# Optimization experiments

Measured on AMD Instinct MI355X. Metric: run time of the kernel, lower is better.

## Reference

```python
import jax, jax.numpy as jnp
import numpy as np

N = 100000   # nodes
E = 1600000  # edges
IN = 128     # input_dim
H = 64       # hidden_dim
OUT = 2      # output_dim
G = 64       # number of graphs in the batch


def setup_inputs() -> dict:
    key = jax.random.key(0)
    ks = jax.random.split(key, 12)
    x = jax.random.normal(ks[0], (N, IN), dtype=jnp.float32)
    edge_index = jax.random.randint(ks[1], (2, E), 0, N, dtype=jnp.int64)
    batch = jnp.sort(jax.random.randint(ks[2], (N,), 0, G, dtype=jnp.int64))
    s = 0.05
    return {
        "x": x,
        "edge_index": edge_index,
        "batch": batch,
        "W1": jax.random.normal(ks[3], (IN, H), dtype=jnp.float32) * s,
        "b1": jnp.zeros((H,), dtype=jnp.float32),
        "W2": jax.random.normal(ks[4], (H, H), dtype=jnp.float32) * s,
        "b2": jnp.zeros((H,), dtype=jnp.float32),
        "W3": jax.random.normal(ks[5], (H, H), dtype=jnp.float32) * s,
        "b3": jnp.zeros((H,), dtype=jnp.float32),
        "Wm1": jax.random.normal(ks[6], (H, H), dtype=jnp.float32) * s,
        "bm1": jnp.zeros((H,), dtype=jnp.float32),
        "Wm2": jax.random.normal(ks[7], (H, OUT), dtype=jnpp.float32) * s if False else jax.random.normal(ks[7], (H, OUT), dtype=jnp.float32) * s,
        "bm2": jnp.zeros((OUT,), dtype=jnp.float32),
    }


def _gcn_conv(x, W, b, src, dst, norm, n_nodes):
    # PyG GCNConv: h = x @ W; message = norm * h[src]; scatter-add at dst; + bias
    h = x @ W                                  # [N, H]
    msg = h[src] * norm[:, None]               # [E+N, H] gather + scale
    out = jax.ops.segment_sum(msg, dst, num_segments=n_nodes)
    return out + b


def reference(x, edge_index, batch, W1, b1, W2, b2, W3, b3, Wm1, bm1, Wm2, bm2):
    n = x.shape[0]
    # add self-loops (PyG GCNConv default add_self_loops=True)
    loop = jnp.arange(n, dtype=edge_index.dtype)
    src = jnp.concatenate([edge_index[0], loop])
    dst = jnp.concatenate([edge_index[1], loop])
    # symmetric normalization deg^-1/2 (deg over target nodes, incl. self-loops)
    deg = jax.ops.segment_sum(jnp.ones_like(dst, dtype=x.dtype), dst, num_segments=n)
    dinv = jnp.where(deg > 0, jax.lax.rsqrt(deg), 0.0)
    norm = dinv[src] * dinv[dst]               # [E+N]

    h = jax.nn.relu(_gcn_conv(x, W1, b1, src, dst, norm, n))   # dropout: eval -> identity
    h = jax.nn.relu(_gcn_conv(h, W2, b2, src, dst, norm, n))
    h = jax.nn.relu(_gcn_conv(h, W3, b3, src, dst, norm, n))

    # global_mean_pool over batch ids
    sums = jax.ops.segment_sum(h, batch, num_segments=G)       # [G, H]
    cnts = jax.ops.segment_sum(jnp.ones((n,), dtype=h.dtype), batch, num_segments=G)
    pooled = sums / jnp.maximum(cnts, 1.0)[:, None]

    # MLP head: Linear -> ReLU -> (Dropout eval) -> Linear
    z = jax.nn.relu(pooled @ Wm1 + bm1)
    return z @ Wm2 + bm2                                       # [G, OUT]
```

## Files before the change

kernel.cpp:

```cpp
#include <hip/hip_runtime.h>
#include <hip/hip_bf16.h>

#define NNODES 100000
#define NEDGES 1600000
#define IND 128
#define HD 64
#define OUTD 2
#define NG 64
#define BINSHIFT 9
#define BINSZ 512
#define BSTRIDE 12288
#define PB 256

typedef __attribute__((ext_vector_type(8))) short short8v;
typedef __attribute__((ext_vector_type(4))) float floatx4;

static __device__ __forceinline__ unsigned short f2bf(float f) {
    __hip_bfloat16 h = __float2bfloat16(f);
    return *(unsigned short*)&h;
}
static __device__ __forceinline__ float bf2f(unsigned short u) {
    __hip_bfloat16 h = *(__hip_bfloat16*)&u;
    return __bfloat162float(h);
}

__global__ __launch_bounds__(1024) void binP_kernel(const int* __restrict__ src,
                                                    const int* __restrict__ dst,
                                                    int* __restrict__ binCount,
                                                    unsigned int* __restrict__ binned,
                                                    int E, int nbins) {
    __shared__ int lh[256];
    __shared__ int lbase[256];
    int t = threadIdx.x;
    if (t < 256) lh[t] = 0;
    __syncthreads();
    int ebpb = (E + PB - 1) / PB;
    int e0 = blockIdx.x * ebpb;
    int e1 = min(e0 + ebpb, E);
    int dcache[8];
    int ec = 0;
    for (int e = e0 + t; e < e1; e += 1024) {
        int d = dst[e];
        dcache[ec++] = d;
        atomicAdd(&lh[d >> BINSHIFT], 1);
    }
    __syncthreads();
    if (t < nbins) {
        int c = lh[t];
        if (c > 0) lbase[t] = atomicAdd(&binCount[t], c);
        lh[t] = 0;
    }
    __syncthreads();
    ec = 0;
    for (int e = e0 + t; e < e1; e += 1024) {
        int d = dcache[ec++];
        int b = d >> BINSHIFT;
        int idx = atomicAdd(&lh[b], 1);
        binned[(size_t)b * BSTRIDE + lbase[b] + idx] =
            ((unsigned int)(d & (BINSZ - 1)) << 17) | (unsigned int)src[e];
    }
}

__global__ __launch_bounds__(1024) void binHD_kernel(const unsigned int* __restrict__ binned,
                                                     const int* __restrict__ binCount,
                                                     float* __restrict__ dinv,
                                                     unsigned int* __restrict__ rowinfo,
                                                     int* __restrict__ ssrc, int n) {
    __shared__ int dh[BINSZ];
    __shared__ int rp[BINSZ];
    __shared__ int wsum[4];
    int b = blockIdx.x, t = threadIdx.x;
    int lane = t & 63, wv = t >> 6;
    if (t < BINSZ) dh[t] = 0;
    __syncthreads();
    int s0 = b * BSTRIDE;
    int cnt = binCount[b];
    for (int i = t; i < cnt; i += 1024)
        atomicAdd(&dh[binned[s0 + i] >> 17], 1);
    __syncthreads();
    if (t < BINSZ) {
        int node = (b << BINSHIFT) + t;
        if (node < n) dinv[node] = 1.0f / sqrtf((float)(dh[t] + 1));
    }
    int d0 = 0, d1 = 0, p = 0;
    if (t < 256) { d0 = dh[2 * t]; d1 = dh[2 * t + 1]; p = d0 + d1; }
    int sc = p;
#pragma unroll
    for (int d = 1; d < 64; d <<= 1) { int v = __shfl_up(sc, d, 64); if (lane >= d) sc += v; }
    if (t < 256 && lane == 63) wsum[wv] = sc;
    __syncthreads();
    if (t < 256) {
        int add = 0;
        for (int w2 = 0; w2 < wv; w2++) add += wsum[w2];
        int ex = sc - p + add;
        rp[2 * t]     = ex;
        rp[2 * t + 1] = ex + d0;
    }
    __syncthreads();
    if (t < BINSZ) {
        int node = (b << BINSHIFT) + t;
        if (node < n)
            rowinfo[node] = ((unsigned int)(s0 + rp[t]) << 10) |
                            (unsigned int)min(dh[t], 1023);
    }
    __syncthreads();
    for (int i = t; i < cnt; i += 1024) {
        unsigned int rec = binned[s0 + i];
        int doff = rec >> 17;
        int s = rec & 0x1FFFF;
        int idx = atomicSub(&dh[doff], 1) - 1;
        ssrc[s0 + rp[doff] + idx] = s;
    }
}

__global__ __launch_bounds__(256) void prep_kernel(const float* __restrict__ W1,
                                                   const float* __restrict__ W2,
                                                   const float* __restrict__ W3,
                                                   unsigned short* __restrict__ WT1,
                                                   unsigned short* __restrict__ WT2,
                                                   unsigned short* __restrict__ WT3,
                                                   const int* __restrict__ batch,
                                                   float* __restrict__ gcnt, int n) {
    int blk = blockIdx.x;
    if (blk < 64) {
        int i = blk * 256 + threadIdx.x;
        if (i < 64 * IND) {
            int nn2 = i / IND, k = i - nn2 * IND;
            WT1[i] = f2bf(W1[k * 64 + nn2]);
        } else if (i < 64 * IND + 64 * HD) {
            int j = i - 64 * IND;
            int nn2 = j / HD, k = j - nn2 * HD;
            WT2[j] = f2bf(W2[k * 64 + nn2]);
        } else {
            int j = i - 64 * IND - 64 * HD;
            int nn2 = j / HD, k = j - nn2 * HD;
            WT3[j] = f2bf(W3[k * 64 + nn2]);
        }
    } else {
        __shared__ float lg[NG];
        int t = threadIdx.x;
        if (t < NG) lg[t] = 0.f;
        __syncthreads();
        int nb2 = gridDim.x - 64;
        int per = (n + nb2 - 1) / nb2;
        int i0 = (blk - 64) * per;
        int i1 = min(i0 + per, n);
        for (int i = i0 + t; i < i1; i += 256)
            atomicAdd(&lg[batch[i]], 1.f);
        __syncthreads();
        if (t < NG) atomicAdd(&gcnt[t], lg[t]);
    }
}

template <int K, bool BF16IN>
__global__ __launch_bounds__(256) void mm_mfma_kernel(const void* __restrict__ Xv,
                                                      const unsigned short* __restrict__ WT,
                                                      const float* __restrict__ dinv,
                                                      unsigned short* __restrict__ Tb, int nn) {
    const int lane = threadIdx.x & 63;
    const int wv   = threadIdx.x >> 6;
    const int nb   = blockIdx.x * 64 + wv * 16;
    if (nb >= nn) return;
    const int col  = lane & 15;
    const int quad = lane >> 4;
    const int m    = min(nb + col, nn - 1);

    floatx4 acc0 = {0.f, 0.f, 0.f, 0.f};
    floatx4 acc1 = {0.f, 0.f, 0.f, 0.f};
    floatx4 acc2 = {0.f, 0.f, 0.f, 0.f};
    floatx4 acc3 = {0.f, 0.f, 0.f, 0.f};

#pragma unroll
    for (int ks = 0; ks < K; ks += 32) {
        const int k0 = ks + quad * 8;
        short8v a;
        if (BF16IN) {
            a = *(const short8v*)((const unsigned short*)Xv + (size_t)m * K + k0);
        } else {
            const float* xr = (const float*)Xv + (size_t)m * K + k0;
            float4 f0 = *(const float4*)(xr);
            float4 f1 = *(const float4*)(xr + 4);
            a[0] = (short)f2bf(f0.x); a[1] = (short)f2bf(f0.y);
            a[2] = (short)f2bf(f0.z); a[3] = (short)f2bf(f0.w);
            a[4] = (short)f2bf(f1.x); a[5] = (short)f2bf(f1.y);
            a[6] = (short)f2bf(f1.z); a[7] = (short)f2bf(f1.w);
        }
        short8v b0 = *(const short8v*)(WT + (size_t)(0  + col) * K + k0);
        short8v b1 = *(const short8v*)(WT + (size_t)(16 + col) * K + k0);
        short8v b2 = *(const short8v*)(WT + (size_t)(32 + col) * K + k0);
        short8v b3 = *(const short8v*)(WT + (size_t)(48 + col) * K + k0);
        acc0 = __builtin_amdgcn_mfma_f32_16x16x32_bf16(a, b0, acc0, 0, 0, 0);
        acc1 = __builtin_amdgcn_mfma_f32_16x16x32_bf16(a, b1, acc1, 0, 0, 0);
        acc2 = __builtin_amdgcn_mfma_f32_16x16x32_bf16(a, b2, acc2, 0, 0, 0);
        acc3 = __builtin_amdgcn_mfma_f32_16x16x32_bf16(a, b3, acc3, 0, 0, 0);
    }

#pragma unroll
    for (int r = 0; r < 4; r++) {
        int node = nb + quad * 4 + r;
        if (node < nn) {
            float sc = dinv[node];
            unsigned short* o = Tb + (size_t)node * 64 + col;
            o[0]  = f2bf(sc * acc0[r]);
            o[16] = f2bf(sc * acc1[r]);
            o[32] = f2bf(sc * acc2[r]);
            o[48] = f2bf(sc * acc3[r]);
        }
    }
}

__global__ __launch_bounds__(256) void agg_kernel(const unsigned short* __restrict__ Tb,
                                                  const unsigned int* __restrict__ rowinfo,
                                                  const int* __restrict__ ssrc,
                                                  const float* __restrict__ dinv,
                                                  const float* __restrict__ bias,
                                                  unsigned short* __restrict__ Ob, int nn) {
    int wave = __builtin_amdgcn_readfirstlane((blockIdx.x * 256 + threadIdx.x) >> 6);
    int lane = threadIdx.x & 63;
    if (wave >= nn) return;
    int n = wave;
    float acc = bf2f(Tb[(size_t)n * 64 + lane]);
    unsigned int info = rowinfo[n];
    int rb = (int)(info >> 10);
    int re = rb + (int)(info & 1023);
    int i = rb;
    for (; i + 16 <= re; i += 16) {
        int s[16];
#pragma unroll
        for (int k = 0; k < 16; k++) s[k] = ssrc[i + k];
        float v[16];
#pragma unroll
        for (int k = 0; k < 16; k++) v[k] = bf2f(Tb[(size_t)s[k] * 64 + lane]);
#pragma unroll
        for (int k = 0; k < 16; k++) acc += v[k];
    }
    for (; i + 4 <= re; i += 4) {
        int s0 = ssrc[i], s1 = ssrc[i + 1], s2 = ssrc[i + 2], s3 = ssrc[i + 3];
        float v0 = bf2f(Tb[(size_t)s0 * 64 + lane]);
        float v1 = bf2f(Tb[(size_t)s1 * 64 + lane]);
        float v2 = bf2f(Tb[(size_t)s2 * 64 + lane]);
        float v3 = bf2f(Tb[(size_t)s3 * 64 + lane]);
        acc += v0; acc += v1; acc += v2; acc += v3;
    }
    for (; i < re; i++)
        acc += bf2f(Tb[(size_t)ssrc[i] * 64 + lane]);
    float o = dinv[n] * acc + bias[lane];
    o = o > 0.f ? o : 0.f;
    Ob[(size_t)n * 64 + lane] = f2bf(o);
}

__global__ __launch_bounds__(256) void pool_kernel(const unsigned short* __restrict__ Hb,
                                                   const int* __restrict__ batch,
                                                   float* __restrict__ pooled, int nn) {
    int wid = (blockIdx.x * 256 + threadIdx.x) >> 6;
    int lane = threadIdx.x & 63;
    int nwaves = (gridDim.x * 256) >> 6;
    int per = (nn + nwaves - 1) / nwaves;
    int n0 = wid * per;
    int n1 = n0 + per; if (n1 > nn) n1 = nn;
    if (n0 >= n1) return;
    int cur = batch[n0];
    float acc = 0.f;
    for (int n = n0; n < n1; ++n) {
        int g = batch[n];
        if (g != cur) {
            atomicAdd(&pooled[cur * 64 + lane], acc);
            acc = 0.f; cur = g;
        }
        acc += bf2f(Hb[(size_t)n * 64 + lane]);
    }
    atomicAdd(&pooled[cur * 64 + lane], acc);
}

__global__ __launch_bounds__(256) void head_kernel(const float* __restrict__ pooled,
                                                   const float* __restrict__ gcnt,
                                                   const float* __restrict__ Wm1,
                                                   const float* __restrict__ bm1,
                                                   const float* __restrict__ Wm2,
                                                   const float* __restrict__ bm2,
                                                   float* __restrict__ out) {
    __shared__ float P[NG * 64];
    __shared__ float Z[NG * 64];
    int tid = threadIdx.x;
    for (int i = tid; i < NG * 64; i += 256) {
        int g = i >> 6;
        float c = gcnt[g];
        c = c > 1.f ? c : 1.f;
        P[i] = pooled[i] / c;
    }
    __syncthreads();
    for (int i = tid; i < NG * 64; i += 256) {
        int g = i >> 6, j = i & 63;
        float a = bm1[j];
#pragma unroll 8
        for (int k = 0; k < 64; ++k) a += P[g * 64 + k] * Wm1[k * 64 + j];
        Z[i] = a > 0.f ? a : 0.f;
    }
    __syncthreads();
    for (int i = tid; i < NG * OUTD; i += 256) {
        int g = i / OUTD, o = i % OUTD;
        float a = bm2[o];
#pragma unroll 8
        for (int k = 0; k < 64; ++k) a += Z[g * 64 + k] * Wm2[k * OUTD + o];
        out[i] = a;
    }
}

extern "C" void kernel_launch(void* const* d_in, const int* in_sizes, int n_in,
                              void* d_out, int out_size, void* d_ws, size_t ws_size,
                              hipStream_t stream) {
    const float* x    = (const float*)d_in[0];
    const int*  edge  = (const int*)d_in[1];
    const int*  batch = (const int*)d_in[2];
    const float* W1 = (const float*)d_in[3];
    const float* b1 = (const float*)d_in[4];
    const float* W2 = (const float*)d_in[5];
    const float* b2 = (const float*)d_in[6];
    const float* W3 = (const float*)d_in[7];
    const float* b3 = (const float*)d_in[8];
    const float* Wm1 = (const float*)d_in[9];
    const float* bm1 = (const float*)d_in[10];
    const float* Wm2 = (const float*)d_in[11];
    const float* bm2 = (const float*)d_in[12];

    const int N_ = in_sizes[2];
    const int E_ = in_sizes[1] / 2;
    const int* src = edge;
    const int* dst = edge + E_;
    const int nbins = (N_ + BINSZ - 1) >> BINSHIFT;

    char* w = (char*)d_ws;
    auto alloc = [&](size_t bytes) -> void* {
        void* p = (void*)w;
        w += (bytes + 255) & ~(size_t)255;
        return p;
    };
    float* dinv   = (float*)alloc((size_t)N_ * 4);
    unsigned int* rowinfo = (unsigned int*)alloc((size_t)N_ * 4);
    float* pooled = (float*)alloc((size_t)(NG * 64 + NG) * 4);
    int*   binCount = (int*)alloc(256 * 4);
    float* gcnt   = pooled + NG * 64;
    int*   ssrc   = (int*)alloc((size_t)nbins * BSTRIDE * 4);
    unsigned int* binned = (unsigned int*)alloc((size_t)nbins * BSTRIDE * 4);
    unsigned short* Tb  = (unsigned short*)alloc((size_t)N_ * 64 * 2);
    unsigned short* hBb = (unsigned short*)alloc((size_t)N_ * 64 * 2);
    unsigned short* WT1 = (unsigned short*)alloc((size_t)64 * IND * 2);
    unsigned short* WT2 = (unsigned short*)alloc((size_t)64 * HD * 2);
    unsigned short* WT3 = (unsigned short*)alloc((size_t)64 * HD * 2);

    hipMemsetAsync(pooled, 0, (size_t)(NG * 64 + NG) * 4 + 256 * 4 + 256, stream);

    binP_kernel<<<PB, 1024, 0, stream>>>(src, dst, binCount, binned, E_, nbins);
    binHD_kernel<<<nbins, 1024, 0, stream>>>(binned, binCount, dinv, rowinfo, ssrc, N_);

    prep_kernel<<<64 + 16, 256, 0, stream>>>(W1, W2, W3, WT1, WT2, WT3, batch, gcnt, N_);

    const int mmblk = (N_ + 63) / 64;
    const int aggblk = (N_ + 3) / 4;

    mm_mfma_kernel<IND, false><<<mmblk, 256, 0, stream>>>(x, WT1, dinv, Tb, N_);
    agg_kernel<<<aggblk, 256, 0, stream>>>(Tb, rowinfo, ssrc, dinv, b1, hBb, N_);
    mm_mfma_kernel<HD, true><<<mmblk, 256, 0, stream>>>(hBb, WT2, dinv, Tb, N_);
    agg_kernel<<<aggblk, 256, 0, stream>>>(Tb, rowinfo, ssrc, dinv, b2, hBb, N_);
    mm_mfma_kernel<HD, true><<<mmblk, 256, 0, stream>>>(hBb, WT3, dinv, Tb, N_);
    agg_kernel<<<aggblk, 256, 0, stream>>>(Tb, rowinfo, ssrc, dinv, b3, hBb, N_);

    pool_kernel<<<256, 256, 0, stream>>>(hBb, batch, pooled, N_);
    head_kernel<<<1, 256, 0, stream>>>(pooled, gcnt, Wm1, bm1, Wm2, bm2, (float*)d_out);
}
```

Baseline: 383.6 us.

## Fuse prep into binning, pool into last aggregation, pack GEMM stores

Folds the weight-transpose and graph-count prep work into extra blocks of the binning kernel, and removes the separate pool kernel by having the final aggregation atomically add each node's output into the pooled sums. It also stages each bin's edge records in LDS during CSR construction, pads per-row offsets to multiples of four, and remaps MFMA output columns so each lane writes four adjacent bf16 values with one 8-byte store. The goal is fewer launches and fewer global reads and writes. The trade-off is that per-node global float atomics onto only 64x64 pooled addresses may contend heavily and make the summation order nondeterministic.

```diff
diff --git a/kernel.cpp b/kernel.cpp
--- a/kernel.cpp
+++ b/kernel.cpp
@@ -28,14 +28,55 @@
                                                     const int* __restrict__ dst,
                                                     int* __restrict__ binCount,
                                                     unsigned int* __restrict__ binned,
-                                                    int E, int nbins) {
+                                                    int E, int nbins,
+                                                    const float* __restrict__ W1,
+                                                    const float* __restrict__ W2,
+                                                    const float* __restrict__ W3,
+                                                    unsigned short* __restrict__ WT1,
+                                                    unsigned short* __restrict__ WT2,
+                                                    unsigned short* __restrict__ WT3,
+                                                    const int* __restrict__ batch,
+                                                    float* __restrict__ gcnt, int n) {
+    int blk = blockIdx.x;
+    int t = threadIdx.x;
+    if (blk >= PB) {
+        int pb = blk - PB;
+        if (pb == 0) {
+            for (int i = t; i < 64 * IND + 64 * HD + 64 * HD; i += 1024) {
+                if (i < 64 * IND) {
+                    int nn2 = i / IND, k = i - nn2 * IND;
+                    WT1[i] = f2bf(W1[k * 64 + nn2]);
+                } else if (i < 64 * IND + 64 * HD) {
+                    int j = i - 64 * IND;
+                    int nn2 = j / HD, k = j - nn2 * HD;
+                    WT2[j] = f2bf(W2[k * 64 + nn2]);
+                } else {
+                    int j = i - 64 * IND - 64 * HD;
+                    int nn2 = j / HD, k = j - nn2 * HD;
+                    WT3[j] = f2bf(W3[k * 64 + nn2]);
+                }
+            }
+        } else {
+            __shared__ float lg[NG];
+            if (t < NG) lg[t] = 0.f;
+            __syncthreads();
+            const int nb2 = 19;
+            int per = (n + nb2 - 1) / nb2;
+            int i0 = (pb - 1) * per;
+            int i1 = min(i0 + per, n);
+            for (int i = i0 + t; i < i1; i += 1024)
+                atomicAdd(&lg[batch[i]], 1.f);
+            __syncthreads();
+            if (t < NG) atomicAdd(&gcnt[t], lg[t]);
+        }
+        return;
+    }
     __shared__ int lh[256];
     __shared__ int lbase[256];
-    int t = threadIdx.x;
     if (t < 256) lh[t] = 0;
     __syncthreads();
     int ebpb = (E + PB - 1) / PB;
-    int e0 = blockIdx.x * ebpb;
+    int e0 = blk * ebpb;
     int e1 = min(e0 + ebpb, E);
     int dcache[8];
     int ec = 0;
@@ -69,21 +110,27 @@
     __shared__ int dh[BINSZ];
     __shared__ int rp[BINSZ];
     __shared__ int wsum[4];
+    __shared__ unsigned int ecl[BSTRIDE];
     int b = blockIdx.x, t = threadIdx.x;
     int lane = t & 63, wv = t >> 6;
     if (t < BINSZ) dh[t] = 0;
-    __syncthreads();
     int s0 = b * BSTRIDE;
     int cnt = binCount[b];
+    for (int i = t; i < cnt; i += 1024) ecl[i] = binned[s0 + i];
+    __syncthreads();
     for (int i = t; i < cnt; i += 1024)
-        atomicAdd(&dh[binned[s0 + i] >> 17], 1);
+        atomicAdd(&dh[ecl[i] >> 17], 1);
     __syncthreads();
     if (t < BINSZ) {
         int node = (b << BINSHIFT) + t;
         if (node < n) dinv[node] = 1.0f / sqrtf((float)(dh[t] + 1));
     }
     int d0 = 0, d1 = 0, p = 0;
-    if (t < 256) { d0 = dh[2 * t]; d1 = dh[2 * t + 1]; p = d0 + d1; }
+    if (t < 256) {
+        d0 = (dh[2 * t] + 3) & ~3;
+        d1 = (dh[2 * t + 1] + 3) & ~3;
+        p = d0 + d1;
+    }
     int sc = p;
 #pragma unroll
     for (int d = 1; d < 64; d <<= 1) { int v = __shfl_up(sc, d, 64); if (lane >= d) sc += v; }
@@ -105,50 +152,11 @@
     }
     __syncthreads();
     for (int i = t; i < cnt; i += 1024) {
-        unsigned int rec = binned[s0 + i];
+        unsigned int rec = ecl[i];
         int doff = rec >> 17;
         int s = rec & 0x1FFFF;
         int idx = atomicSub(&dh[doff], 1) - 1;
         ssrc[s0 + rp[doff] + idx] = s;
-    }
-}
-
-__global__ __launch_bounds__(256) void prep_kernel(const float* __restrict__ W1,
-                                                   const float* __restrict__ W2,
-                                                   const float* __restrict__ W3,
-                                                   unsigned short* __restrict__ WT1,
-                                                   unsigned short* __restrict__ WT2,
-                                                   unsigned short* __restrict__ WT3,
-                                                   const int* __restrict__ batch,
-                                                   float* __restrict__ gcnt, int n) {
-    int blk = blockIdx.x;
-    if (blk < 64) {
-        int i = blk * 256 + threadIdx.x;
-        if (i < 64 * IND) {
-            int nn2 = i / IND, k = i - nn2 * IND;
-            WT1[i] = f2bf(W1[k * 64 + nn2]);
-        } else if (i < 64 * IND + 64 * HD) {
-            int j = i - 64 * IND;
-            int nn2 = j / HD, k = j - nn2 * HD;
-            WT2[j] = f2bf(W2[k * 64 + nn2]);
-        } else {
-            int j = i - 64 * IND - 64 * HD;
-            int nn2 = j / HD, k = j - nn2 * HD;
-            WT3[j] = f2bf(W3[k * 64 + nn2]);
-        }
-    } else {
-        __shared__ float lg[NG];
-        int t = threadIdx.x;
-        if (t < NG) lg[t] = 0.f;
-        __syncthreads();
-        int nb2 = gridDim.x - 64;
-        int per = (n + nb2 - 1) / nb2;
-        int i0 = (blk - 64) * per;
-        int i1 = min(i0 + per, n);
-        for (int i = i0 + t; i < i1; i += 256)
-            atomicAdd(&lg[batch[i]], 1.f);
-        __syncthreads();
-        if (t < NG) atomicAdd(&gcnt[t], lg[t]);
     }
 }
 
@@ -185,10 +193,10 @@
             a[4] = (short)f2bf(f1.x); a[5] = (short)f2bf(f1.y);
             a[6] = (short)f2bf(f1.z); a[7] = (short)f2bf(f1.w);
         }
-        short8v b0 = *(const short8v*)(WT + (size_t)(0  + col) * K + k0);
-        short8v b1 = *(const short8v*)(WT + (size_t)(16 + col) * K + k0);
-        short8v b2 = *(const short8v*)(WT + (size_t)(32 + col) * K + k0);
-        short8v b3 = *(const short8v*)(WT + (size_t)(48 + col) * K + k0);
+        short8v b0 = *(const short8v*)(WT + (size_t)(4 * col + 0) * K + k0);
+        short8v b1 = *(const short8v*)(WT + (size_t)(4 * col + 1) * K + k0);
+        short8v b2 = *(const short8v*)(WT + (size_t)(4 * col + 2) * K + k0);
+        short8v b3 = *(const short8v*)(WT + (size_t)(4 * col + 3) * K + k0);
         acc0 = __builtin_amdgcn_mfma_f32_16x16x32_bf16(a, b0, acc0, 0, 0, 0);
         acc1 = __builtin_amdgcn_mfma_f32_16x16x32_bf16(a, b1, acc1, 0, 0, 0);
         acc2 = __builtin_amdgcn_mfma_f32_16x16x32_bf16(a, b2, acc2, 0, 0, 0);
@@ -200,21 +208,25 @@
         int node = nb + quad * 4 + r;
         if (node < nn) {
             float sc = dinv[node];
-            unsigned short* o = Tb + (size_t)node * 64 + col;
-            o[0]  = f2bf(sc * acc0[r]);
-            o[16] = f2bf(sc * acc1[r]);
-            o[32] = f2bf(sc * acc2[r]);
-            o[48] = f2bf(sc * acc3[r]);
+            unsigned int lo = (unsigned int)f2bf(sc * acc0[r]) |
+                              ((unsigned int)f2bf(sc * acc1[r]) << 16);
+            unsigned int hi = (unsigned int)f2bf(sc * acc2[r]) |
+                              ((unsigned int)f2bf(sc * acc3[r]) << 16);
+            uint2 st; st.x = lo; st.y = hi;
+            ((uint2*)Tb)[(size_t)node * 16 + col] = st;
         }
     }
 }
 
+template <int POOL>
 __global__ __launch_bounds__(256) void agg_kernel(const unsigned short* __restrict__ Tb,
                                                   const unsigned int* __restrict__ rowinfo,
                                                   const int* __restrict__ ssrc,
                                                   const float* __restrict__ dinv,
                                                   const float* __restrict__ bias,
-                                                  unsigned short* __restrict__ Ob, int nn) {
+                                                  unsigned short* __restrict__ Ob,
+                                                  const int* __restrict__ batch,
+                                                  float* __restrict__ pooled, int nn) {
     int wave = __builtin_amdgcn_readfirstlane((blockIdx.x * 256 + threadIdx.x) >> 6);
     int lane = threadIdx.x & 63;
     if (wave >= nn) return;
@@ -246,30 +258,11 @@
         acc += bf2f(Tb[(size_t)ssrc[i] * 64 + lane]);
     float o = dinv[n] * acc + bias[lane];
     o = o > 0.f ? o : 0.f;
-    Ob[(size_t)n * 64 + lane] = f2bf(o);
-}
-
-__global__ __launch_bounds__(256) void pool_kernel(const unsigned short* __restrict__ Hb,
-                                                   const int* __restrict__ batch,
-                                                   float* __restrict__ pooled, int nn) {
-    int wid = (blockIdx.x * 256 + threadIdx.x) >> 6;
-    int lane = threadIdx.x & 63;
-    int nwaves = (gridDim.x * 256) >> 6;
-    int per = (nn + nwaves - 1) / nwaves;
-    int n0 = wid * per;
-    int n1 = n0 + per; if (n1 > nn) n1 = nn;
-    if (n0 >= n1) return;
-    int cur = batch[n0];
-    float acc = 0.f;
-    for (int n = n0; n < n1; ++n) {
-        int g = batch[n];
-        if (g != cur) {
-            atomicAdd(&pooled[cur * 64 + lane], acc);
-            acc = 0.f; cur = g;
-        }
-        acc += bf2f(Hb[(size_t)n * 64 + lane]);
-    }
-    atomicAdd(&pooled[cur * 64 + lane], acc);
+    if (POOL) {
+        atomicAdd(&pooled[batch[n] * 64 + lane], o);
+    } else {
+        Ob[(size_t)n * 64 + lane] = f2bf(o);
+    }
 }
 
 __global__ __launch_bounds__(256) void head_kernel(const float* __restrict__ pooled,
@@ -350,21 +343,19 @@
 
     hipMemsetAsync(pooled, 0, (size_t)(NG * 64 + NG) * 4 + 256 * 4 + 256, stream);
 
-    binP_kernel<<<PB, 1024, 0, stream>>>(src, dst, binCount, binned, E_, nbins);
+    binP_kernel<<<PB + 20, 1024, 0, stream>>>(src, dst, binCount, binned, E_, nbins,
+                                              W1, W2, W3, WT1, WT2, WT3, batch, gcnt, N_);
     binHD_kernel<<<nbins, 1024, 0, stream>>>(binned, binCount, dinv, rowinfo, ssrc, N_);
-
-    prep_kernel<<<64 + 16, 256, 0, stream>>>(W1, W2, W3, WT1, WT2, WT3, batch, gcnt, N_);
 
     const int mmblk = (N_ + 63) / 64;
     const int aggblk = (N_ + 3) / 4;
 
     mm_mfma_kernel<IND, false><<<mmblk, 256, 0, stream>>>(x, WT1, dinv, Tb, N_);
-    agg_kernel<<<aggblk, 256, 0, stream>>>(Tb, rowinfo, ssrc, dinv, b1, hBb, N_);
+    agg_kernel<0><<<aggblk, 256, 0, stream>>>(Tb, rowinfo, ssrc, dinv, b1, hBb, batch, pooled, N_);
     mm_mfma_kernel<HD, true><<<mmblk, 256, 0, stream>>>(hBb, WT2, dinv, Tb, N_);
-    agg_kernel<<<aggblk, 256, 0, stream>>>(Tb, rowinfo, ssrc, dinv, b2, hBb, N_);
+    agg_kernel<0><<<aggblk, 256, 0, stream>>>(Tb, rowinfo, ssrc, dinv, b2, hBb, batch, pooled, N_);
     mm_mfma_kernel<HD, true><<<mmblk, 256, 0, stream>>>(hBb, WT3, dinv, Tb, N_);
-    agg_kernel<<<aggblk, 256, 0, stream>>>(Tb, rowinfo, ssrc, dinv, b3, hBb, N_);
-
-    pool_kernel<<<256, 256, 0, stream>>>(hBb, batch, pooled, N_);
+    agg_kernel<1><<<aggblk, 256, 0, stream>>>(Tb, rowinfo, ssrc, dinv, b3, hBb, batch, pooled, N_);
+
     head_kernel<<<1, 256, 0, stream>>>(pooled, gcnt, Wm1, bm1, Wm2, bm2, (float*)d_out);
 }
```

Measured after the change: 453.2 us. 1.18x slower.
